# Kernel tuning notes

Hardware: AMD Instinct MI355X
Metric: run time of the kernel (lower is better)

The kernel has to match this reference:

```python
import jax, jax.numpy as jnp
import numpy as np
from jax import lax

V, H, M, OD, NL, S, B, KS = 32000, 1024, 16, 16, 4, 512, 16, 3
N = H // M          # 64
DN = OD * N         # 1024 (layernorm dim)
EPS = 1e-5


def _layernorm(x, g, b):
    mu = jnp.mean(x, axis=-1, keepdims=True)
    var = jnp.var(x, axis=-1, keepdims=True)
    return (x - mu) * lax.rsqrt(var + EPS) * g + b


def _conv(x, w, b):
    y = lax.conv_general_dilated(x, w, (1, 1), 'SAME',
                                 dimension_numbers=('NCHW', 'OIHW', 'NCHW'))
    return y + b[None, :, None, None]


def setup_inputs() -> dict:
    key = jax.random.key(0)
    ks = jax.random.split(key, 16)
    inp = {
        'x': jax.random.randint(ks[0], (B, S), 0, V),
        'emb_table': jax.random.normal(ks[1], (V, H), jnp.float32) * 0.02,
        'ln0_g': jnp.ones((H,), jnp.float32),
        'ln0_b': jnp.zeros((H,), jnp.float32),
        'qw': jax.random.normal(ks[2], (NL, OD, M, KS, KS), jnp.float32) * 0.05,
        'qb': jnp.zeros((NL, OD), jnp.float32),
        'kw': jax.random.normal(ks[3], (NL, OD, M, KS, KS), jnp.float32) * 0.05,
        'kb': jnp.zeros((NL, OD), jnp.float32),
        'vw': jax.random.normal(ks[4], (NL, OD, M, KS, KS), jnp.float32) * 0.05,
        'vb': jnp.zeros((NL, OD), jnp.float32),
        'lng': jnp.ones((NL, DN), jnp.float32),
        'lnb': jnp.zeros((NL, DN), jnp.float32),
        'cw': jax.random.normal(ks[5], (NL, M, OD, 3, 3), jnp.float32) * 0.05,
        'cb': jnp.zeros((NL, M), jnp.float32),
    }
    return inp


def reference(x, emb_table, ln0_g, ln0_b, qw, qb, kw, kb, vw, vb, lng, lnb, cw, cb):
    gelu = lambda t: jax.nn.gelu(t, approximate=False)  # torch nn.GELU default (erf)
    # embedding with padding_idx=0 (row forced to zero)
    table = emb_table.at[0].set(0.0)
    h = _layernorm(table[x], ln0_g, ln0_b)              # [B,S,H]
    h = h.reshape(B, S, M, N).transpose(0, 2, 1, 3)      # [B,M,S,N]
    outs = ()
    for i in range(NL):
        outs = outs + (h,)
        q = gelu(_conv(h, qw[i], qb[i]))                 # [B,OD,S,N]
        k = gelu(_conv(h, kw[i], kb[i]))
        v = gelu(_conv(h, vw[i], vb[i]))
        q2 = q.transpose(0, 2, 1, 3).reshape(B, S, DN)   # [B,S,OD*N]
        k2 = k.transpose(0, 1, 3, 2).reshape(B, DN, S)   # [B,OD*N,S]
        v2 = v.transpose(0, 2, 1, 3).reshape(B, S, DN)
        score = jax.nn.softmax(jnp.matmul(q2, k2), axis=0)  # softmax over batch (dim=0)
        o = jnp.matmul(score, v2)                        # [B,S,DN]
        o = _layernorm(o, lng[i], lnb[i])
        o = o.reshape(B, S, OD, N).transpose(0, 2, 1, 3)  # [B,OD,S,N]
        h = gelu(_conv(o, cw[i], cb[i])) + h             # residual, [B,M,S,N]
    return (h,) + outs
```

## Files before the change

kernel.cpp:

```cpp
#include <hip/hip_runtime.h>
#include <hip/hip_bf16.h>

typedef unsigned short u16;
typedef unsigned int   u32;
typedef short bf16x8 __attribute__((ext_vector_type(8)));
typedef float f32x4  __attribute__((ext_vector_type(4)));

#define SS 512
#define XSWZ(g) ((((g) & 7) << 6) | ((g) >> 3))
#define WPREP_STRIDE 22016

__device__ __forceinline__ float gelu_f(float v){
    float x  = v * 0.70710678118654752f;
    float ax = fabsf(x);
    float t  = __builtin_amdgcn_rcpf(fmaf(0.3275911f, ax, 1.0f));
    float poly = t*(0.254829592f + t*(-0.284496736f + t*(1.421413741f
               + t*(-1.453152027f + t*1.061405429f))));
    float e  = __expf(-x*x);
    float er = copysignf(1.0f - poly*e, x);
    return 0.5f*v*(1.0f + er);
}
__device__ __forceinline__ u16 bf16_rne(float v){
    u32 u = __float_as_uint(v);
    u32 r = u + 0x7FFF + ((u >> 16) & 1);
    return (u16)(r >> 16);
}
#define DYT(t) ((t)>=9 ? 0 : (t)/3)
#define DXT(t) ((t)>=9 ? 0 : (t)%3)

__global__ __launch_bounds__(256) void k_prep(
    const float* __restrict__ qw, const float* __restrict__ kw,
    const float* __restrict__ vw, const float* __restrict__ cw,
    const float* __restrict__ lng, const float* __restrict__ lnb,
    u16* __restrict__ wprep)
{
    int L = blockIdx.x;
    int tid = threadIdx.x;
    u16* base = wprep + L*WPREP_STRIDE;
    const float* src[4] = {qw + L*2304, kw + L*2304, vw + L*2304, cw + L*2304};
    const int offh[4] = {0, 5120, 10240, 12800};
    const int offl[4] = {2560, 7680, -1, 15360};
    for (int idx = tid; idx < 2304; idx += 256){
        int o = idx / 144, rem = idx - o*144;
        int i = rem / 9, tap = rem - i*9;
        int dst = o*160 + tap*16 + i;
        #pragma unroll
        for (int a = 0; a < 4; ++a){
            float wv = src[a][idx];
            u16 hv = bf16_rne(wv);
            base[offh[a] + dst] = hv;
            if (offl[a] >= 0)
                base[offl[a] + dst] = bf16_rne(wv - __uint_as_float((u32)hv<<16));
        }
    }
    {
        int o = tid >> 4, kk = tid & 15;
        int d = o*160 + 144 + kk;
        base[d]=0; base[2560+d]=0; base[5120+d]=0; base[7680+d]=0;
        base[10240+d]=0; base[12800+d]=0; base[15360+d]=0;
    }
    float* gr = (float*)(base + 17920);
    float* br = (float*)(base + 19968);
    for (int idx = tid; idx < 1024; idx += 256){
        int od = (idx & 15)*64 + (idx >> 4);
        gr[idx] = lng[L*1024 + od];
        br[idx] = lnb[L*1024 + od];
    }
}

__global__ __launch_bounds__(256) void k_embed_ln(
    const int* __restrict__ x, const float* __restrict__ emb,
    const float* __restrict__ g, const float* __restrict__ bta,
    float* __restrict__ h, u16* __restrict__ hh, u16* __restrict__ hl)
{
    int bs = blockIdx.x;
    int b = bs >> 9, s = bs & 511;
    int t = x[bs];
    int tid = threadIdx.x;
    float v[4];
    #pragma unroll
    for (int j = 0; j < 4; ++j){
        int idx = tid + j*256;
        v[j] = (t == 0) ? 0.0f : emb[(size_t)t*1024 + idx];
    }
    float sum = v[0]+v[1]+v[2]+v[3];
    float sq  = v[0]*v[0]+v[1]*v[1]+v[2]*v[2]+v[3]*v[3];
    __shared__ float red[2][4];
    int lane = tid & 63, wid = tid >> 6;
    #pragma unroll
    for (int off = 32; off; off >>= 1){
        sum += __shfl_down(sum, off, 64);
        sq  += __shfl_down(sq,  off, 64);
    }
    if (lane == 0){ red[0][wid] = sum; red[1][wid] = sq; }
    __syncthreads();
    sum = red[0][0]+red[0][1]+red[0][2]+red[0][3];
    sq  = red[1][0]+red[1][1]+red[1][2]+red[1][3];
    float mean = sum * (1.0f/1024.0f);
    float var  = sq  * (1.0f/1024.0f) - mean*mean;
    float rs = rsqrtf(var + 1e-5f);
    #pragma unroll
    for (int j = 0; j < 4; ++j){
        int idx = tid + j*256;
        float y = (v[j]-mean)*rs*g[idx] + bta[idx];
        int m = idx >> 6, n = idx & 63;
        h[((size_t)(b*16 + m)*SS + s)*64 + n] = y;
        u16 hv = bf16_rne(y);
        u16 lv = bf16_rne(y - __uint_as_float((u32)hv<<16));
        size_t da = ((size_t)b*SS + s)*1024 + n*16 + m;
        hh[da] = hv; hl[da] = lv;
    }
}

__global__ __launch_bounds__(512,1) void k_conv_qkv(
    const u16* __restrict__ inh, const u16* __restrict__ inl,
    const u16* __restrict__ wp,
    const float* __restrict__ qb, const float* __restrict__ kb,
    const float* __restrict__ vb,
    u16* __restrict__ qoh, u16* __restrict__ qol,
    u16* __restrict__ koh, u16* __restrict__ kol,
    u16* __restrict__ vT)
{
    int bid = XSWZ(blockIdx.x);
    int b  = bid >> 5;
    int y0 = (bid & 31) * 16;
    int tid = threadIdx.x;
    int w8 = tid >> 6, lane = tid & 63;
    int l15 = lane & 15, l4 = lane >> 4;
    int xt = w8 & 3, yh8 = (w8 >> 2) * 8;

    __shared__ __align__(16) u16 wq_h[2560], wq_l[2560], wk_h[2560], wk_l[2560], wv_h[2560];
    __shared__ u16 shi[18*68*24];
    __shared__ u16 slo[18*68*24];

    if (tid < 320){
        ((uint4*)wq_h)[tid] = ((const uint4*)(wp        ))[tid];
        ((uint4*)wq_l)[tid] = ((const uint4*)(wp +  2560))[tid];
        ((uint4*)wk_h)[tid] = ((const uint4*)(wp +  5120))[tid];
        ((uint4*)wk_l)[tid] = ((const uint4*)(wp +  7680))[tid];
        ((uint4*)wv_h)[tid] = ((const uint4*)(wp + 10240))[tid];
    }
    if (tid < 72){
        int y = tid >> 2, rr = tid & 3;
        int tc = (rr >> 1) ? 65 : 0;
        int h8 = (rr & 1) * 8;
        int ad = (y*68 + tc)*24 + h8;
        *(uint4*)&shi[ad] = make_uint4(0,0,0,0);
        *(uint4*)&slo[ad] = make_uint4(0,0,0,0);
    }
    for (int idx = tid; idx < 2304; idx += 512){
        int y = idx >> 7;
        int rem = idx & 127;
        int xx = rem >> 1, h8 = (rem & 1)*8;
        int gy = y0 - 1 + y;
        uint4 vh = make_uint4(0,0,0,0), vl = make_uint4(0,0,0,0);
        if (gy >= 0 && gy < SS){
            size_t ga = ((size_t)b*SS + gy)*1024 + xx*16 + h8;
            vh = *(const uint4*)(inh + ga);
            vl = *(const uint4*)(inl + ga);
        }
        int la = (y*68 + (xx+1))*24 + h8;
        *(uint4*)&shi[la] = vh;
        *(uint4*)&slo[la] = vl;
    }
    __syncthreads();

    bf16x8 aq_h[5], aq_l[5], ak_h[5], ak_l[5], av_h[5];
    #pragma unroll
    for (int p = 0; p < 5; ++p){
        int aad = l15*160 + p*32 + l4*8;
        aq_h[p] = *(const bf16x8*)&wq_h[aad];
        aq_l[p] = *(const bf16x8*)&wq_l[aad];
        ak_h[p] = *(const bf16x8*)&wk_h[aad];
        ak_l[p] = *(const bf16x8*)&wk_l[aad];
        av_h[p] = *(const bf16x8*)&wv_h[aad];
    }

    f32x4 accq[8], acck[8], accv[8];
    #pragma unroll
    for (int i = 0; i < 8; ++i){
        accq[i] = (f32x4){0.f,0.f,0.f,0.f};
        acck[i] = (f32x4){0.f,0.f,0.f,0.f};
        accv[i] = (f32x4){0.f,0.f,0.f,0.f};
    }
    int hsel = l4 >> 1;
    int i0 = (l4 & 1)*8;
    int xo = xt*16 + l15;

    #pragma unroll
    for (int p = 0; p < 5; ++p){
        int dy = hsel ? DYT(2*p+1) : DYT(2*p);
        int dx = hsel ? DXT(2*p+1) : DXT(2*p);
        int badd0 = ((dy + yh8)*68 + xo + dx)*24 + i0;
        #pragma unroll
        for (int yy = 0; yy < 8; ++yy){
            int bad = badd0 + yy*(68*24);
            bf16x8 bh = *(const bf16x8*)&shi[bad];
            bf16x8 bl = *(const bf16x8*)&slo[bad];
            accq[yy] = __builtin_amdgcn_mfma_f32_16x16x32_bf16(aq_h[p], bh, accq[yy],0,0,0);
            accq[yy] = __builtin_amdgcn_mfma_f32_16x16x32_bf16(aq_l[p], bh, accq[yy],0,0,0);
            accq[yy] = __builtin_amdgcn_mfma_f32_16x16x32_bf16(aq_h[p], bl, accq[yy],0,0,0);
            acck[yy] = __builtin_amdgcn_mfma_f32_16x16x32_bf16(ak_h[p], bh, acck[yy],0,0,0);
            acck[yy] = __builtin_amdgcn_mfma_f32_16x16x32_bf16(ak_l[p], bh, acck[yy],0,0,0);
            acck[yy] = __builtin_amdgcn_mfma_f32_16x16x32_bf16(ak_h[p], bl, acck[yy],0,0,0);
            accv[yy] = __builtin_amdgcn_mfma_f32_16x16x32_bf16(av_h[p], bh, accv[yy],0,0,0);
        }
    }

    float qbv[4], kbv[4], vbv[4];
    #pragma unroll
    for (int i = 0; i < 4; ++i){
        qbv[i] = qb[l4*4 + i];
        kbv[i] = kb[l4*4 + i];
        vbv[i] = vb[l4*4 + i];
    }
    union { u16 u[4][8]; uint4 q[4]; } vpk;
    #pragma unroll
    for (int yy = 0; yy < 8; ++yy){
        int y = y0 + yh8 + yy;
        u16 qh4[4], ql4[4], kh4[4], kl4[4];
        #pragma unroll
        for (int i = 0; i < 4; ++i){
            float vq = gelu_f(accq[yy][i] + qbv[i]);
            u16 hv = bf16_rne(vq);
            qh4[i] = hv; ql4[i] = bf16_rne(vq - __uint_as_float((u32)hv<<16));
            float vk = gelu_f(acck[yy][i] + kbv[i]);
            u16 kv = bf16_rne(vk);
            kh4[i] = kv; kl4[i] = bf16_rne(vk - __uint_as_float((u32)kv<<16));
            vpk.u[i][yy] = bf16_rne(gelu_f(accv[yy][i] + vbv[i]));
        }
        size_t oa = ((size_t)b*SS + y)*1024 + xo*16 + l4*4;
        *(uint2*)&qoh[oa] = make_uint2((u32)qh4[0]|((u32)qh4[1]<<16),(u32)qh4[2]|((u32)qh4[3]<<16));
        *(uint2*)&qol[oa] = make_uint2((u32)ql4[0]|((u32)ql4[1]<<16),(u32)ql4[2]|((u32)ql4[3]<<16));
        *(uint2*)&koh[oa] = make_uint2((u32)kh4[0]|((u32)kh4[1]<<16),(u32)kh4[2]|((u32)kh4[3]<<16));
        *(uint2*)&kol[oa] = make_uint2((u32)kl4[0]|((u32)kl4[1]<<16),(u32)kl4[2]|((u32)kl4[3]<<16));
    }
    #pragma unroll
    for (int i = 0; i < 4; ++i)
        *(uint4*)(vT + ((size_t)b*1024 + xo*16 + l4*4 + i)*SS + y0 + yh8) = vpk.q[i];
}

__global__ __launch_bounds__(512,1) void k_conv_ln_res2(
    const float* __restrict__ o_pre, const float* __restrict__ stats,
    const u16* __restrict__ wp, const float* __restrict__ bias,
    const float* __restrict__ resid, float* __restrict__ outf,
    u16* __restrict__ outh, u16* __restrict__ outl)
{
    int bid = XSWZ(blockIdx.x);
    int b  = bid >> 5;
    int y0 = (bid & 31) * 16;
    int tid = threadIdx.x;
    int w8 = tid >> 6, lane = tid & 63;
    int l15 = lane & 15, l4 = lane >> 4;
    int xt = w8 & 3, yh8 = (w8 >> 2) * 8;

    __shared__ __align__(16) u16 whi[2560], wlo[2560];
    __shared__ u16 shi[18*68*24], slo[18*68*24];
    __shared__ __align__(16) float grem[1024], brem[1024];
    __shared__ float smu[18], srs[18];

    if (tid < 320){
        ((uint4*)whi)[tid] = ((const uint4*)(wp + 12800))[tid];
        ((uint4*)wlo)[tid] = ((const uint4*)(wp + 15360))[tid];
    }
    if (tid < 256){
        ((float4*)grem)[tid] = ((const float4*)(wp + 17920))[tid];
        ((float4*)brem)[tid] = ((const float4*)(wp + 19968))[tid];
    }
    if (tid < 18){
        int gy = y0 - 1 + tid;
        float mu = 0.f, rs = 0.f;
        if (gy >= 0 && gy < SS){
            float s = stats[2*((size_t)b*SS + gy)];
            float q = stats[2*((size_t)b*SS + gy) + 1];
            mu = s * (1.0f/1024.0f);
            float var = q * (1.0f/1024.0f) - mu*mu;
            rs = rsqrtf(var + 1e-5f);
        }
        smu[tid] = mu; srs[tid] = rs;
    }
    if (tid >= 64 && tid < 136){
        int t2 = tid - 64;
        int y = t2 >> 2, rr = t2 & 3;
        int tc = (rr >> 1) ? 65 : 0;
        int h8 = (rr & 1) * 8;
        int ad = (y*68 + tc)*24 + h8;
        *(uint4*)&shi[ad] = make_uint4(0,0,0,0);
        *(uint4*)&slo[ad] = make_uint4(0,0,0,0);
    }
    __syncthreads();

    for (int idx = tid; idx < 4608; idx += 512){
        int y = idx >> 8;
        int rem = idx & 255;
        int xx = rem >> 2, cq = (rem & 3)*4;
        int gy = y0 - 1 + y;
        int la = (y*68 + xx + 1)*24 + cq;
        if (gy >= 0 && gy < SS){
            float4 vv = *(const float4*)(o_pre + ((size_t)b*SS + gy)*1024 + xx*16 + cq);
            float mu = smu[y], rs = srs[y];
            int dbase = xx*16 + cq;
            float va[4] = {vv.x, vv.y, vv.z, vv.w};
            u16 hh4[4], ll4[4];
            #pragma unroll
            for (int j = 0; j < 4; ++j){
                float yv = (va[j] - mu)*rs*grem[dbase + j] + brem[dbase + j];
                hh4[j] = bf16_rne(yv);
                ll4[j] = bf16_rne(yv - __uint_as_float((u32)hh4[j]<<16));
            }
            *(uint2*)&shi[la] = make_uint2((u32)hh4[0]|((u32)hh4[1]<<16),(u32)hh4[2]|((u32)hh4[3]<<16));
            *(uint2*)&slo[la] = make_uint2((u32)ll4[0]|((u32)ll4[1]<<16),(u32)ll4[2]|((u32)ll4[3]<<16));
        } else {
            *(uint2*)&shi[la] = make_uint2(0,0);
            *(uint2*)&slo[la] = make_uint2(0,0);
        }
    }
    __syncthreads();

    bf16x8 ah[5], al[5];
    #pragma unroll
    for (int p = 0; p < 5; ++p){
        int aad = l15*160 + p*32 + l4*8;
        ah[p] = *(const bf16x8*)&whi[aad];
        al[p] = *(const bf16x8*)&wlo[aad];
    }

    f32x4 acc[8];
    #pragma unroll
    for (int i = 0; i < 8; ++i) acc[i] = (f32x4){0.f,0.f,0.f,0.f};
    int hsel = l4 >> 1;
    int i0 = (l4 & 1)*8;
    int xo = xt*16 + l15;

    #pragma unroll
    for (int p = 0; p < 5; ++p){
        int dy = hsel ? DYT(2*p+1) : DYT(2*p);
        int dx = hsel ? DXT(2*p+1) : DXT(2*p);
        int badd0 = ((dy + yh8)*68 + xo + dx)*24 + i0;
        #pragma unroll
        for (int yy = 0; yy < 8; ++yy){
            int bad = badd0 + yy*(68*24);
            bf16x8 bh = *(const bf16x8*)&shi[bad];
            bf16x8 bl = *(const bf16x8*)&slo[bad];
            acc[yy] = __builtin_amdgcn_mfma_f32_16x16x32_bf16(ah[p], bh, acc[yy],0,0,0);
            acc[yy] = __builtin_amdgcn_mfma_f32_16x16x32_bf16(al[p], bh, acc[yy],0,0,0);
            acc[yy] = __builtin_amdgcn_mfma_f32_16x16x32_bf16(ah[p], bl, acc[yy],0,0,0);
        }
    }

    float bv[4];
    #pragma unroll
    for (int i = 0; i < 4; ++i) bv[i] = bias[l4*4 + i];
    #pragma unroll
    for (int yy = 0; yy < 8; ++yy){
        int y = y0 + yh8 + yy;
        float r[4];
        #pragma unroll
        for (int i = 0; i < 4; ++i) r[i] = gelu_f(acc[yy][i] + bv[i]);
        #pragma unroll
        for (int i = 0; i < 4; ++i){
            int o = l4*4 + i;
            size_t fa = ((size_t)(b*16 + o)*SS + y)*64 + xo;
            float hv = resid[fa] + r[i];
            outf[fa] = hv;
            r[i] = hv;
        }
        u16 hh_[4], ll_[4];
        #pragma unroll
        for (int i = 0; i < 4; ++i){
            hh_[i] = bf16_rne(r[i]);
            ll_[i] = bf16_rne(r[i] - __uint_as_float((u32)hh_[i]<<16));
        }
        size_t oa = ((size_t)b*SS + y)*1024 + xo*16 + l4*4;
        *(uint2*)&outh[oa] = make_uint2((u32)hh_[0]|((u32)hh_[1]<<16),(u32)hh_[2]|((u32)hh_[3]<<16));
        *(uint2*)&outl[oa] = make_uint2((u32)ll_[0]|((u32)ll_[1]<<16),(u32)ll_[2]|((u32)ll_[3]<<16));
    }
}

__global__ __launch_bounds__(256) void k_qk_mfma(
    const u16* __restrict__ qh, const u16* __restrict__ ql,
    const u16* __restrict__ kh, const u16* __restrict__ kl,
    float* __restrict__ score)
{
    int bid = XSWZ(blockIdx.x);
    int b = bid >> 5;
    int s1_0 = ((bid >> 3) & 3) * 128;
    int s2_0 = (bid & 7) * 64;
    __shared__ u16 Ah[128*64], Al[128*64], Bh[64*64], Bl[64*64];
    int tid = threadIdx.x;
    int w = tid >> 6, lane = tid & 63;
    int l15 = lane & 15, l4 = lane >> 4;
    f32x4 acc[2][4];
    #pragma unroll
    for (int r=0;r<2;++r)
        #pragma unroll
        for(int c=0;c<4;++c) acc[r][c] = (f32x4){0.f,0.f,0.f,0.f};

    for (int oc = 0; oc < 16; ++oc){
        size_t qbase = ((size_t)b*SS + s1_0)*1024 + oc*64;
        size_t kbase = ((size_t)b*SS + s2_0)*1024 + oc*64;
        #pragma unroll
        for (int i = 0; i < 4; ++i){
            int idx = tid + i*256;
            int r = idx >> 3, f = idx & 7;
            int dst = r*64 + ((f ^ (r & 7))*8);
            *(uint4*)&Ah[dst] = *(const uint4*)(qh + qbase + (size_t)r*1024 + f*8);
            *(uint4*)&Al[dst] = *(const uint4*)(ql + qbase + (size_t)r*1024 + f*8);
        }
        #pragma unroll
        for (int i = 0; i < 2; ++i){
            int idx = tid + i*256;
            int r = idx >> 3, f = idx & 7;
            int dst = r*64 + ((f ^ (r & 7))*8);
            *(uint4*)&Bh[dst] = *(const uint4*)(kh + kbase + (size_t)r*1024 + f*8);
            *(uint4*)&Bl[dst] = *(const uint4*)(kl + kbase + (size_t)r*1024 + f*8);
        }
        __syncthreads();
        #pragma unroll
        for (int ks = 0; ks < 2; ++ks){
            bf16x8 a_h[2], a_l[2];
            #pragma unroll
            for (int r=0;r<2;++r){
                int row = w*32 + r*16 + l15;
                int ad = row*64 + (((ks*4 + l4) ^ (row & 7))*8);
                a_h[r] = *(const bf16x8*)&Ah[ad];
                a_l[r] = *(const bf16x8*)&Al[ad];
            }
            #pragma unroll
            for (int c=0;c<4;++c){
                int row = c*16 + l15;
                int bd = row*64 + (((ks*4 + l4) ^ (row & 7))*8);
                bf16x8 b_h = *(const bf16x8*)&Bh[bd];
                bf16x8 b_l = *(const bf16x8*)&Bl[bd];
                #pragma unroll
                for (int r=0;r<2;++r){
                    acc[r][c] = __builtin_amdgcn_mfma_f32_16x16x32_bf16(a_h[r], b_h, acc[r][c],0,0,0);
                    acc[r][c] = __builtin_amdgcn_mfma_f32_16x16x32_bf16(a_l[r], b_h, acc[r][c],0,0,0);
                    acc[r][c] = __builtin_amdgcn_mfma_f32_16x16x32_bf16(a_h[r], b_l, acc[r][c],0,0,0);
                }
            }
        }
        __syncthreads();
    }
    #pragma unroll
    for (int r=0;r<2;++r)
        #pragma unroll
        for (int c=0;c<4;++c)
            #pragma unroll
            for (int i=0;i<4;++i){
                int s1 = s1_0 + w*32 + r*16 + l4*4 + i;
                int s2 = s2_0 + c*16 + l15;
                score[((size_t)b*SS + s1)*SS + s2] = acc[r][c][i];
            }
}

__global__ __launch_bounds__(256) void k_softmax_b(
    const float* __restrict__ score, u16* __restrict__ scb,
    float* __restrict__ stats)
{
    int sid = blockIdx.x*256 + threadIdx.x;
    if (sid < 16384) stats[sid] = 0.0f;
    float vals[16];
    float m = -1e30f;
    #pragma unroll
    for (int b = 0; b < 16; ++b){
        vals[b] = score[(size_t)b*SS*SS + sid];
        m = fmaxf(m, vals[b]);
    }
    float sum = 0.f;
    #pragma unroll
    for (int b = 0; b < 16; ++b){ vals[b] = __expf(vals[b]-m); sum += vals[b]; }
    float inv = 1.0f/sum;
    #pragma unroll
    for (int b = 0; b < 16; ++b) scb[(size_t)b*SS*SS + sid] = bf16_rne(vals[b]*inv);
}

__global__ __launch_bounds__(256) void k_sv_mfma(
    const u16* __restrict__ scb, const u16* __restrict__ vT,
    float* __restrict__ o, float* __restrict__ stats)
{
    int bid = XSWZ(blockIdx.x);
    int b = bid >> 5;
    int s1_0 = ((bid >> 3) & 3) * 128;
    int d0 = (bid & 7) * 128;
    __shared__ u16 As[128*64], Bs[128*64];
    int tid = threadIdx.x;
    int w = tid >> 6, lane = tid & 63;
    int l15 = lane & 15, l4 = lane >> 4;
    f32x4 acc[2][8];
    #pragma unroll
    for (int r=0;r<2;++r)
        #pragma unroll
        for(int c=0;c<8;++c) acc[r][c] = (f32x4){0.f,0.f,0.f,0.f};

    for (int st = 0; st < 8; ++st){
        int s2b = st*64;
        #pragma unroll
        for (int i = 0; i < 4; ++i){
            int idx = tid + i*256;
            int r = idx >> 3, f = idx & 7;
            int dst = r*64 + ((f ^ (r & 7))*8);
            *(uint4*)&As[dst] = *(const uint4*)(scb + ((size_t)b*SS + s1_0 + r)*SS + s2b + f*8);
            *(uint4*)&Bs[dst] = *(const uint4*)(vT + ((size_t)b*1024 + d0 + r)*SS + s2b + f*8);
        }
        __syncthreads();
        #pragma unroll
        for (int ks = 0; ks < 2; ++ks){
            bf16x8 a0[2];
            #pragma unroll
            for (int r=0;r<2;++r){
                int row = w*32 + r*16 + l15;
                a0[r] = *(const bf16x8*)&As[row*64 + (((ks*4 + l4) ^ (row & 7))*8)];
            }
            #pragma unroll
            for (int c=0;c<8;++c){
                int row = c*16 + l15;
                bf16x8 b0 = *(const bf16x8*)&Bs[row*64 + (((ks*4 + l4) ^ (row & 7))*8)];
                #pragma unroll
                for (int r=0;r<2;++r)
                    acc[r][c] = __builtin_amdgcn_mfma_f32_16x16x32_bf16(a0[r], b0, acc[r][c],0,0,0);
            }
        }
        __syncthreads();
    }
    #pragma unroll
    for (int r=0;r<2;++r)
        #pragma unroll
        for (int c=0;c<8;++c)
            #pragma unroll
            for (int i=0;i<4;++i){
                int s1 = s1_0 + w*32 + r*16 + l4*4 + i;
                o[((size_t)b*SS + s1)*1024 + d0 + c*16 + l15] = acc[r][c][i];
            }

    #pragma unroll
    for (int r=0;r<2;++r){
        #pragma unroll
        for (int i=0;i<4;++i){
            float s = 0.f, q = 0.f;
            #pragma unroll
            for (int c=0;c<8;++c){ float v = acc[r][c][i]; s += v; q += v*v; }
            #pragma unroll
            for (int m = 1; m <= 8; m <<= 1){
                s += __shfl_xor(s, m, 64);
                q += __shfl_xor(q, m, 64);
            }
            if (l15 == 0){
                int s1 = s1_0 + w*32 + r*16 + l4*4 + i;
                atomicAdd(&stats[2*((size_t)b*SS + s1)],     s);
                atomicAdd(&stats[2*((size_t)b*SS + s1) + 1], q);
            }
        }
    }
}

extern "C" void kernel_launch(void* const* d_in, const int* in_sizes, int n_in,
                              void* d_out, int out_size, void* d_ws, size_t ws_size,
                              hipStream_t stream)
{
    const int*   x    = (const int*)  d_in[0];
    const float* emb  = (const float*)d_in[1];
    const float* g0   = (const float*)d_in[2];
    const float* b0   = (const float*)d_in[3];
    const float* qw   = (const float*)d_in[4];
    const float* qb   = (const float*)d_in[5];
    const float* kw   = (const float*)d_in[6];
    const float* kb   = (const float*)d_in[7];
    const float* vw   = (const float*)d_in[8];
    const float* vb_  = (const float*)d_in[9];
    const float* lng  = (const float*)d_in[10];
    const float* lnb  = (const float*)d_in[11];
    const float* cw   = (const float*)d_in[12];
    const float* cb   = (const float*)d_in[13];
    float* out = (float*)d_out;

    const size_t TS = (size_t)16*16*512*64;
    u16* wsu = (u16*)d_ws;
    u16* hh = wsu + 0*TS;
    u16* hl = wsu + 1*TS;
    u16* qh = wsu + 2*TS;
    u16* ql = wsu + 3*TS;
    u16* kh = wsu + 4*TS;
    u16* kl = wsu + 5*TS;
    u16* vT = wsu + 6*TS;
    float* sc    = (float*)(wsu + 7*TS);
    u16*   scb   = qh;
    float* o_pre = (float*)(wsu + 4*TS);
    float* stats = (float*)(wsu + 3*TS);
    u16* wprep = (u16*)((char*)d_ws + ((size_t)160 << 20));

    float* hbuf[5];
    hbuf[0] = out + 1*TS;
    hbuf[1] = out + 2*TS;
    hbuf[2] = out + 3*TS;
    hbuf[3] = out + 4*TS;
    hbuf[4] = out;

    k_prep<<<4, 256, 0, stream>>>(qw, kw, vw, cw, lng, lnb, wprep);
    k_embed_ln<<<8192, 256, 0, stream>>>(x, emb, g0, b0, hbuf[0], hh, hl);
    for (int i = 0; i < 4; ++i){
        const u16* wp = wprep + i*WPREP_STRIDE;
        k_conv_qkv<<<512, 512, 0, stream>>>(
            hh, hl, wp, qb + i*16, kb + i*16, vb_ + i*16, qh, ql, kh, kl, vT);
        k_qk_mfma<<<512, 256, 0, stream>>>(qh, ql, kh, kl, sc);
        k_softmax_b<<<1024, 256, 0, stream>>>(sc, scb, stats);
        k_sv_mfma<<<512, 256, 0, stream>>>(scb, vT, o_pre, stats);
        k_conv_ln_res2<<<512, 512, 0, stream>>>(
            o_pre, stats, wp, cb + i*16, hbuf[i], hbuf[i+1], hh, hl);
    }
}
```

Before: 592.0 us.

## Split QKV conv into smaller 8-row tiles and read weights from global

The QKV convolution kernel now launches 1024 blocks of 256 threads, each covering 8 output rows instead of 16, with launch bounds raised to allow two blocks per CU. The staged input tile shrinks to 10 halo rows, cutting shared memory per block. Weight fragments are loaded straight from global memory into registers, dropping the shared-memory weight staging and its copy. The goal is more resident blocks and less LDS pressure, paid for with a larger halo overhead (10 rows loaded per 8 computed) and repeated global weight reads.

```diff
diff --git a/kernel.cpp b/kernel.cpp
--- a/kernel.cpp
+++ b/kernel.cpp
@@ -7,7 +7,8 @@
 typedef float f32x4  __attribute__((ext_vector_type(4)));
 
 #define SS 512
-#define XSWZ(g) ((((g) & 7) << 6) | ((g) >> 3))
+#define XSWZ(g)     ((((g) & 7) << 6) | ((g) >> 3))
+#define XSWZ1024(g) ((((g) & 7) << 7) | ((g) >> 3))
 #define WPREP_STRIDE 22016
 
 __device__ __forceinline__ float gelu_f(float v){
@@ -112,7 +113,7 @@
     }
 }
 
-__global__ __launch_bounds__(512,1) void k_conv_qkv(
+__global__ __launch_bounds__(256,2) void k_conv_qkv(
     const u16* __restrict__ inh, const u16* __restrict__ inl,
     const u16* __restrict__ wp,
     const float* __restrict__ qb, const float* __restrict__ kb,
@@ -121,26 +122,17 @@
     u16* __restrict__ koh, u16* __restrict__ kol,
     u16* __restrict__ vT)
 {
-    int bid = XSWZ(blockIdx.x);
-    int b  = bid >> 5;
-    int y0 = (bid & 31) * 16;
+    int bid = XSWZ1024(blockIdx.x);
+    int b  = bid >> 6;
+    int y0 = (bid & 63) * 8;
     int tid = threadIdx.x;
-    int w8 = tid >> 6, lane = tid & 63;
+    int w4 = tid >> 6, lane = tid & 63;
     int l15 = lane & 15, l4 = lane >> 4;
-    int xt = w8 & 3, yh8 = (w8 >> 2) * 8;
-
-    __shared__ __align__(16) u16 wq_h[2560], wq_l[2560], wk_h[2560], wk_l[2560], wv_h[2560];
-    __shared__ u16 shi[18*68*24];
-    __shared__ u16 slo[18*68*24];
-
-    if (tid < 320){
-        ((uint4*)wq_h)[tid] = ((const uint4*)(wp        ))[tid];
-        ((uint4*)wq_l)[tid] = ((const uint4*)(wp +  2560))[tid];
-        ((uint4*)wk_h)[tid] = ((const uint4*)(wp +  5120))[tid];
-        ((uint4*)wk_l)[tid] = ((const uint4*)(wp +  7680))[tid];
-        ((uint4*)wv_h)[tid] = ((const uint4*)(wp + 10240))[tid];
-    }
-    if (tid < 72){
+
+    __shared__ u16 shi[10*68*24];
+    __shared__ u16 slo[10*68*24];
+
+    if (tid < 40){
         int y = tid >> 2, rr = tid & 3;
         int tc = (rr >> 1) ? 65 : 0;
         int h8 = (rr & 1) * 8;
@@ -148,7 +140,9 @@
         *(uint4*)&shi[ad] = make_uint4(0,0,0,0);
         *(uint4*)&slo[ad] = make_uint4(0,0,0,0);
     }
-    for (int idx = tid; idx < 2304; idx += 512){
+    #pragma unroll
+    for (int it = 0; it < 5; ++it){
+        int idx = tid + it*256;
         int y = idx >> 7;
         int rem = idx & 127;
         int xx = rem >> 1, h8 = (rem & 1)*8;
@@ -169,11 +163,11 @@
     #pragma unroll
     for (int p = 0; p < 5; ++p){
         int aad = l15*160 + p*32 + l4*8;
-        aq_h[p] = *(const bf16x8*)&wq_h[aad];
-        aq_l[p] = *(const bf16x8*)&wq_l[aad];
-        ak_h[p] = *(const bf16x8*)&wk_h[aad];
-        ak_l[p] = *(const bf16x8*)&wk_l[aad];
-        av_h[p] = *(const bf16x8*)&wv_h[aad];
+        aq_h[p] = *(const bf16x8*)&wp[aad];
+        aq_l[p] = *(const bf16x8*)&wp[2560 + aad];
+        ak_h[p] = *(const bf16x8*)&wp[5120 + aad];
+        ak_l[p] = *(const bf16x8*)&wp[7680 + aad];
+        av_h[p] = *(const bf16x8*)&wp[10240 + aad];
     }
 
     f32x4 accq[8], acck[8], accv[8];
@@ -185,13 +179,13 @@
     }
     int hsel = l4 >> 1;
     int i0 = (l4 & 1)*8;
-    int xo = xt*16 + l15;
+    int xo = w4*16 + l15;
 
     #pragma unroll
     for (int p = 0; p < 5; ++p){
         int dy = hsel ? DYT(2*p+1) : DYT(2*p);
         int dx = hsel ? DXT(2*p+1) : DXT(2*p);
-        int badd0 = ((dy + yh8)*68 + xo + dx)*24 + i0;
+        int badd0 = (dy*68 + xo + dx)*24 + i0;
         #pragma unroll
         for (int yy = 0; yy < 8; ++yy){
             int bad = badd0 + yy*(68*24);
@@ -217,7 +211,7 @@
     union { u16 u[4][8]; uint4 q[4]; } vpk;
     #pragma unroll
     for (int yy = 0; yy < 8; ++yy){
-        int y = y0 + yh8 + yy;
+        int y = y0 + yy;
         u16 qh4[4], ql4[4], kh4[4], kl4[4];
         #pragma unroll
         for (int i = 0; i < 4; ++i){
@@ -237,7 +231,7 @@
     }
     #pragma unroll
     for (int i = 0; i < 4; ++i)
-        *(uint4*)(vT + ((size_t)b*1024 + xo*16 + l4*4 + i)*SS + y0 + yh8) = vpk.q[i];
+        *(uint4*)(vT + ((size_t)b*1024 + xo*16 + l4*4 + i)*SS + y0) = vpk.q[i];
 }
 
 __global__ __launch_bounds__(512,1) void k_conv_ln_res2(
@@ -600,7 +594,7 @@
     k_embed_ln<<<8192, 256, 0, stream>>>(x, emb, g0, b0, hbuf[0], hh, hl);
     for (int i = 0; i < 4; ++i){
         const u16* wp = wprep + i*WPREP_STRIDE;
-        k_conv_qkv<<<512, 512, 0, stream>>>(
+        k_conv_qkv<<<1024, 256, 0, stream>>>(
             hh, hl, wp, qb + i*16, kb + i*16, vb_ + i*16, qh, ql, kh, kl, vT);
         k_qk_mfma<<<512, 256, 0, stream>>>(qh, ql, kh, kl, sc);
         k_softmax_b<<<1024, 256, 0, stream>>>(sc, scb, stats);
```

Result: faster. 579.4 us (-2.1%).
